# Performance work log

Hardware: AMD Instinct MI355X
Metric: run time of the kernel (lower is better)

Reference implementation:

```python
import jax, jax.numpy as jnp
import numpy as np

B, L, D, H = 4, 1024, 1024, 16
DH = D // H
NEG = -1e9


def setup_inputs() -> dict:
    key = jax.random.key(0)
    ks = jax.random.split(key, 8)
    sequence = jax.random.normal(ks[0], (B, L, D), dtype=jnp.float32)
    # additive padding mask: all tokens valid -> zeros
    padding_mask = jnp.zeros((B, 1, 1, L), dtype=jnp.float32)
    # additive causal dependency mask: -1e9 above the diagonal
    causal = jnp.triu(jnp.full((L, L), NEG, dtype=jnp.float32), k=1)
    dependency_mask = causal[None, None, :, :]
    scale = 1.0 / np.sqrt(D)
    Wq = jax.random.normal(ks[1], (D, D), dtype=jnp.float32) * scale
    Wk = jax.random.normal(ks[2], (D, D), dtype=jnp.float32) * scale
    Wv = jax.random.normal(ks[3], (D, D), dtype=jnp.float32) * scale
    bq = jnp.zeros((D,), dtype=jnp.float32)
    bk = jnp.zeros((D,), dtype=jnp.float32)
    bv = jnp.zeros((D,), dtype=jnp.float32)
    return {"sequence": sequence, "padding_mask": padding_mask,
            "dependency_mask": dependency_mask,
            "Wq": Wq, "bq": bq, "Wk": Wk, "bk": bk, "Wv": Wv, "bv": bv}


def reference(sequence, padding_mask, dependency_mask, Wq, bq, Wk, bk, Wv, bv):
    b, l, d = sequence.shape
    h, dh = H, d // H
    # Q/K/V linear projections (torch Linear: x @ W^T + b)
    q = (sequence @ Wq.T + bq).reshape(b, l, h, dh)
    k = (sequence @ Wk.T + bk).reshape(b, l, h, dh)
    v = (sequence @ Wv.T + bv).reshape(b, l, h, dh)
    # scaled dot-product scores: [B, H, L, L]
    scores = jnp.einsum('blhd,bmhd->bhlm', q, k) / jnp.sqrt(jnp.float32(dh))
    scores = scores + padding_mask + dependency_mask
    attn = jax.nn.softmax(scores, axis=-1)
    # dropout is identity in eval mode (training=False)
    out = jnp.einsum('bhlm,bmhd->blhd', attn, v)
    return out.reshape(b, l, d)
```

## Files before the change

kernel.cpp:

```cpp
#include <hip/hip_runtime.h>
#include <hip/hip_bf16.h>


#define LL 1024

typedef __attribute__((ext_vector_type(8))) short short8;
typedef __attribute__((ext_vector_type(4))) float floatx4;

__device__ __forceinline__ float bf2f(unsigned short u) {
    return __uint_as_float(((unsigned int)u) << 16);
}
__device__ __forceinline__ unsigned short f2bf(float f) {
    unsigned int x = __float_as_uint(f);
    unsigned int r = x + 0x7fffu + ((x >> 16) & 1u);
    return (unsigned short)(r >> 16);
}

#if __has_builtin(__builtin_amdgcn_global_load_lds)
#define HAVE_GLL 1
typedef __attribute__((address_space(1))) unsigned int as1_u32;
typedef __attribute__((address_space(3))) unsigned int as3_u32;
__device__ __forceinline__ void gll16(const void* g, void* l) {
    __builtin_amdgcn_global_load_lds((const as1_u32*)g, (as3_u32*)l, 16, 0, 0);
}
#endif

#if __has_builtin(__builtin_amdgcn_exp2f)
#define EXP2F(x) __builtin_amdgcn_exp2f(x)
#else
#define EXP2F(x) exp2f(x)
#endif

__global__ __launch_bounds__(256) void conv_in(
    const float* __restrict__ seq, const float* __restrict__ wq,
    const float* __restrict__ wk,  const float* __restrict__ wv,
    const float* __restrict__ bq,  const float* __restrict__ bk,
    const float* __restrict__ bv,  const float* __restrict__ pm,
    unsigned short* __restrict__ ws)
{
    unsigned int t = blockIdx.x * 256u + threadIdx.x;
    if (t >= 918400u) return;
    unsigned int e = t * 8u;
    const float* src; unsigned int idx; unsigned short* dst; float scale = 1.0f;
    if (e < 4194304u)      { src = seq; idx = e;            dst = ws + 12582912u; }
    else if (e < 5242880u) { src = wq;  idx = e - 4194304u; dst = ws + 16777216u; }
    else if (e < 6291456u) { src = wk;  idx = e - 5242880u; dst = ws + 17825792u; }
    else if (e < 7340032u) { src = wv;  idx = e - 6291456u; dst = ws + 18874368u; }
    else if (e < 7341056u) { src = bq;  idx = e - 7340032u; dst = ws + 20971520u; }
    else if (e < 7342080u) { src = bk;  idx = e - 7341056u; dst = ws + 20972544u; }
    else if (e < 7343104u) { src = bv;  idx = e - 7342080u; dst = ws + 20973568u; }
    else { src = pm; idx = e - 7343104u; dst = ws + 20974592u; scale = 1.4426950f; }
    float4 a = *(const float4*)(src + idx);
    float4 c = *(const float4*)(src + idx + 4);
    uint4 st;
    st.x = (unsigned)f2bf(a.x * scale) | ((unsigned)f2bf(a.y * scale) << 16);
    st.y = (unsigned)f2bf(a.z * scale) | ((unsigned)f2bf(a.w * scale) << 16);
    st.z = (unsigned)f2bf(c.x * scale) | ((unsigned)f2bf(c.y * scale) << 16);
    st.w = (unsigned)f2bf(c.z * scale) | ((unsigned)f2bf(c.w * scale) << 16);
    *(uint4*)(dst + idx) = st;
}

__global__ __launch_bounds__(512, 2) void qkv_proj(
    const unsigned short* __restrict__ X,
    const unsigned short* __restrict__ Wq, const unsigned short* __restrict__ bq,
    const unsigned short* __restrict__ Wk, const unsigned short* __restrict__ bk,
    const unsigned short* __restrict__ Wv, const unsigned short* __restrict__ bv,
    unsigned short* __restrict__ dst_base)
{
    const int z = blockIdx.z;
    const unsigned short* Wm   = (z == 0) ? Wq : ((z == 1) ? Wk : Wv);
    const unsigned short* bias = (z == 0) ? bq : ((z == 1) ? bk : bv);
    const float osc = (z == 0) ? 0.18033688f : 1.0f;
    unsigned short* dst = dst_base + (size_t)z * (4096u * 1024u);

    __shared__ __align__(16) unsigned short Abuf[2][16384];
    __shared__ __align__(16) unsigned short Bbuf[2][16384];

    const int tid  = threadIdx.x;
    const int lane = tid & 63;
    const int wave = tid >> 6;
    const int quad = lane >> 4, r16 = lane & 15;
    const int wr = wave >> 2, wc = wave & 3;
    const int m0 = blockIdx.x * 256;
    const int n0 = blockIdx.y * 256;

    const int r3   = lane >> 3;
    const int stc  = ((lane & 7) ^ r3) << 3;
    const int seg0 = wave * 4;

    const unsigned short* Asrc = X  + (size_t)(m0 + seg0 * 8 + r3) * 1024 + stc;
    const unsigned short* Bsrc = Wm + (size_t)(n0 + seg0 * 8 + r3) * 1024 + stc;

    floatx4 acc[8][4];
#pragma unroll
    for (int i = 0; i < 8; ++i)
#pragma unroll
        for (int j = 0; j < 4; ++j)
#pragma unroll
            for (int r = 0; r < 4; ++r) acc[i][j][r] = 0.f;

#ifdef HAVE_GLL
#pragma unroll
    for (int c = 0; c < 4; ++c) {
        gll16(Asrc + (size_t)c * 8192, &Abuf[0][(seg0 + c) * 512]);
        gll16(Bsrc + (size_t)c * 8192, &Bbuf[0][(seg0 + c) * 512]);
    }
#else
#pragma unroll
    for (int c = 0; c < 4; ++c) {
        *(uint4*)&Abuf[0][(seg0 + c) * 512 + lane * 8] = *(const uint4*)(Asrc + (size_t)c * 8192);
        *(uint4*)&Bbuf[0][(seg0 + c) * 512 + lane * 8] = *(const uint4*)(Bsrc + (size_t)c * 8192);
    }
#endif
    asm volatile("s_waitcnt vmcnt(0) lgkmcnt(0)" ::: "memory");
    __builtin_amdgcn_s_barrier();

#pragma unroll 2
    for (int t = 0; t < 16; ++t) {
        const int cur = t & 1;
        const int nxt = cur ^ 1;
        const int k0n = (t + 1) << 6;
        const unsigned short* Ac = Abuf[cur];
        const unsigned short* Bc = Bbuf[cur];
        const int arow = (wr * 128 + r16) * 64;
        const int brow = (wc * 64 + r16) * 64;
        const int c0 = ((0 + quad) ^ (r16 & 7)) << 3;
        const int c1 = ((4 + quad) ^ (r16 & 7)) << 3;
        short8 a[4], b[4];

#pragma unroll
        for (int i = 0; i < 4; ++i)
            a[i] = *(const short8*)&Ac[arow + i * 1024 + c0];
#pragma unroll
        for (int j = 0; j < 4; ++j)
            b[j] = *(const short8*)&Bc[brow + j * 1024 + c0];
        if (t < 15) {
#ifdef HAVE_GLL
#pragma unroll
            for (int c = 0; c < 4; ++c)
                gll16(Asrc + (size_t)c * 8192 + k0n, &Abuf[nxt][(seg0 + c) * 512]);
#else
#pragma unroll
            for (int c = 0; c < 4; ++c)
                *(uint4*)&Abuf[nxt][(seg0 + c) * 512 + lane * 8] =
                    *(const uint4*)(Asrc + (size_t)c * 8192 + k0n);
#endif
        }
        __builtin_amdgcn_s_barrier();
        asm volatile("s_waitcnt lgkmcnt(0)" ::: "memory");
        __builtin_amdgcn_s_setprio(1);
#pragma unroll
        for (int i = 0; i < 4; ++i)
#pragma unroll
            for (int j = 0; j < 4; ++j)
                acc[i][j] = __builtin_amdgcn_mfma_f32_16x16x32_bf16(a[i], b[j], acc[i][j], 0, 0, 0);
        __builtin_amdgcn_s_setprio(0);
        __builtin_amdgcn_s_barrier();

#pragma unroll
        for (int i = 0; i < 4; ++i)
            a[i] = *(const short8*)&Ac[arow + (4 + i) * 1024 + c0];
        if (t < 15) {
#ifdef HAVE_GLL
#pragma unroll
            for (int c = 0; c < 4; ++c)
                gll16(Bsrc + (size_t)c * 8192 + k0n, &Bbuf[nxt][(seg0 + c) * 512]);
#else
#pragma unroll
            for (int c = 0; c < 4; ++c)
                *(uint4*)&Bbuf[nxt][(seg0 + c) * 512 + lane * 8] =
                    *(const uint4*)(Bsrc + (size_t)c * 8192 + k0n);
#endif
        }
        __builtin_amdgcn_s_barrier();
        asm volatile("s_waitcnt lgkmcnt(0)" ::: "memory");
        __builtin_amdgcn_s_setprio(1);
#pragma unroll
        for (int i = 0; i < 4; ++i)
#pragma unroll
            for (int j = 0; j < 4; ++j)
                acc[4 + i][j] = __builtin_amdgcn_mfma_f32_16x16x32_bf16(a[i], b[j], acc[4 + i][j], 0, 0, 0);
        __builtin_amdgcn_s_setprio(0);
        __builtin_amdgcn_s_barrier();

#pragma unroll
        for (int i = 0; i < 4; ++i)
            a[i] = *(const short8*)&Ac[arow + i * 1024 + c1];
#pragma unroll
        for (int j = 0; j < 4; ++j)
            b[j] = *(const short8*)&Bc[brow + j * 1024 + c1];
        __builtin_amdgcn_s_barrier();
        asm volatile("s_waitcnt lgkmcnt(0)" ::: "memory");
        __builtin_amdgcn_s_setprio(1);
#pragma unroll
        for (int i = 0; i < 4; ++i)
#pragma unroll
            for (int j = 0; j < 4; ++j)
                acc[i][j] = __builtin_amdgcn_mfma_f32_16x16x32_bf16(a[i], b[j], acc[i][j], 0, 0, 0);
        __builtin_amdgcn_s_setprio(0);
        __builtin_amdgcn_s_barrier();

#pragma unroll
        for (int i = 0; i < 4; ++i)
            a[i] = *(const short8*)&Ac[arow + (4 + i) * 1024 + c1];
        __builtin_amdgcn_s_barrier();
        asm volatile("s_waitcnt lgkmcnt(0)" ::: "memory");
        __builtin_amdgcn_s_setprio(1);
#pragma unroll
        for (int i = 0; i < 4; ++i)
#pragma unroll
            for (int j = 0; j < 4; ++j)
                acc[4 + i][j] = __builtin_amdgcn_mfma_f32_16x16x32_bf16(a[i], b[j], acc[4 + i][j], 0, 0, 0);
        __builtin_amdgcn_s_setprio(0);
        if (t < 15) {
            asm volatile("s_waitcnt vmcnt(0) lgkmcnt(0)" ::: "memory");
        }
        __builtin_amdgcn_s_barrier();
    }

#pragma unroll
    for (int j = 0; j < 4; ++j) {
        int n = n0 + wc * 64 + j * 16 + r16;
        float bvf = bf2f(bias[n]);
        int h = n >> 6, d = n & 63;
#pragma unroll
        for (int i = 0; i < 8; ++i) {
            int m_base = m0 + wr * 128 + i * 16 + quad * 4;
            int b = m_base >> 10, l0 = m_base & 1023;
            if (z == 2) {
                ushort4 st;
                st.x = f2bf(acc[i][j][0] + bvf); st.y = f2bf(acc[i][j][1] + bvf);
                st.z = f2bf(acc[i][j][2] + bvf); st.w = f2bf(acc[i][j][3] + bvf);
                *(ushort4*)&dst[(((size_t)(b * 16 + h)) * 64 + d) * 1024 + l0] = st;
            } else {
#pragma unroll
                for (int r = 0; r < 4; ++r)
                    dst[(((size_t)(b * 16 + h)) * 1024 + (l0 + r)) * 64 + d] =
                        f2bf((acc[i][j][r] + bvf) * osc);
            }
        }
    }
}

__global__ __launch_bounds__(256) void attn(
    const unsigned short* __restrict__ Qw,
    const unsigned short* __restrict__ Kw,
    const unsigned short* __restrict__ Vt_g,
    const unsigned short* __restrict__ pmask,
    float* __restrict__ out)
{
    __shared__ __align__(16) unsigned short KsF[8192];
    __shared__ __align__(16) unsigned short VsF[8192];
    __shared__ __align__(16) unsigned short PsF[2][4][2048];

    const int tid  = threadIdx.x;
    const int lane = tid & 63;
    const int wave = tid >> 6;
    const int quad = lane >> 4, r16 = lane & 15;

    const int bid  = blockIdx.x;
    const int half = bid >> 8, idx = bid & 255;
    const int bh   = idx & 63;
    const int qb   = idx >> 6;
    const int qi   = half ? (7 - qb) : qb;
    const int b    = bh >> 4, h = bh & 15;
    const int q0   = qi << 7;

    const size_t base = (size_t)bh * (1024 * 64);
    const unsigned short* Qg = Qw + base;
    const unsigned short* Kg = Kw + base;
    const unsigned short* Vg = Vt_g + base;

    const int kst_r3  = lane >> 3;
    const int kst_col = ((lane & 7) ^ kst_r3) << 3;
    const int vst_r   = lane >> 4;

    short8 aq[2][2];
#pragma unroll
    for (int f = 0; f < 2; ++f) {
        int qrow = q0 + f * 64 + wave * 16 + r16;
        aq[f][0] = *(const short8*)(Qg + (size_t)qrow * 64 + quad * 8);
        aq[f][1] = *(const short8*)(Qg + (size_t)qrow * 64 + 32 + quad * 8);
    }

    short8 ones;
#pragma unroll
    for (int i = 0; i < 8; ++i) ones[i] = (short)0x3f80;

    floatx4 ol[2];
    floatx4 o[2][4];
#pragma unroll
    for (int f = 0; f < 2; ++f)
#pragma unroll
        for (int r = 0; r < 4; ++r) ol[f][r] = 0.f;
#pragma unroll
    for (int f = 0; f < 2; ++f)
#pragma unroll
        for (int j = 0; j < 4; ++j)
#pragma unroll
            for (int r = 0; r < 4; ++r) o[f][j][r] = 0.f;

    for (int kt = 0; kt <= qi; ++kt) {
        float pm2[8];
#pragma unroll
        for (int j = 0; j < 8; ++j)
            pm2[j] = bf2f(pmask[b * LL + kt * 128 + j * 16 + r16]) - 12.0f;

        __syncthreads();
#ifdef HAVE_GLL
#pragma unroll
        for (int c2 = 0; c2 < 4; ++c2) {
            int seg = wave * 4 + c2;
            int krow = seg * 8 + kst_r3;
            gll16(Kg + (size_t)(kt * 128 + krow) * 64 + kst_col, &KsF[seg * 512]);
            int vrow = seg * 4 + vst_r;
            int vcol = (((lane & 15) ^ (vrow & 7))) << 3;
            gll16(Vg + (size_t)vrow * 1024 + kt * 128 + vcol, &VsF[seg * 512]);
        }
#else
#pragma unroll
        for (int c2 = 0; c2 < 4; ++c2) {
            int seg = wave * 4 + c2;
            int krow = seg * 8 + kst_r3;
            *(uint4*)&KsF[seg * 512 + lane * 8] =
                *(const uint4*)(Kg + (size_t)(kt * 128 + krow) * 64 + kst_col);
            int vrow = seg * 4 + vst_r;
            int vcol = (((lane & 15) ^ (vrow & 7))) << 3;
            *(uint4*)&VsF[seg * 512 + lane * 8] =
                *(const uint4*)(Vg + (size_t)vrow * 1024 + kt * 128 + vcol);
        }
#endif
        __syncthreads();

#pragma unroll
        for (int f = 0; f < 2; ++f) {
            floatx4 s[8];
#pragma unroll
            for (int j = 0; j < 8; ++j)
#pragma unroll
                for (int r = 0; r < 4; ++r) s[j][r] = 0.f;
#pragma unroll
            for (int j = 0; j < 8; ++j) {
                short8 bk0 = *(const short8*)&KsF[(j * 16 + r16) * 64 + (((0 * 4 + quad) ^ (r16 & 7)) << 3)];
                s[j] = __builtin_amdgcn_mfma_f32_16x16x32_bf16(aq[f][0], bk0, s[j], 0, 0, 0);
                short8 bk1 = *(const short8*)&KsF[(j * 16 + r16) * 64 + (((1 * 4 + quad) ^ (r16 & 7)) << 3)];
                s[j] = __builtin_amdgcn_mfma_f32_16x16x32_bf16(aq[f][1], bk1, s[j], 0, 0, 0);
            }

            if (kt == qi) {
                const int my_q = q0 + f * 64 + wave * 16 + quad * 4;
#pragma unroll
                for (int j = 0; j < 8; ++j) {
                    int key = kt * 128 + j * 16 + r16;
#pragma unroll
                    for (int r = 0; r < 4; ++r)
                        if (key > my_q + r) s[j][r] -= 1.0e9f;
                }
            }

#pragma unroll
            for (int j = 0; j < 8; ++j) {
                int key = j * 16 + r16;
                int ab = ((key >> 5) << 9) + (((key >> 3) & 3) << 7) + (key & 7) + (quad << 5);
#pragma unroll
                for (int r = 0; r < 4; ++r) {
                    float p = EXP2F(s[j][r] + pm2[j]);
                    PsF[f][wave][ab + (r << 3)] = (unsigned short)(__float_as_uint(p) >> 16);
                }
            }
            asm volatile("s_waitcnt lgkmcnt(0)" ::: "memory");

#pragma unroll
            for (int kk4 = 0; kk4 < 4; ++kk4) {
                short8 ap = *(const short8*)&PsF[f][wave][kk4 * 512 + lane * 8];
                ol[f] = __builtin_amdgcn_mfma_f32_16x16x32_bf16(ap, ones, ol[f], 0, 0, 0);
#pragma unroll
                for (int j2 = 0; j2 < 4; ++j2) {
                    short8 bv = *(const short8*)&VsF[(j2 * 16 + r16) * 128 + (((kk4 * 4 + quad) ^ (r16 & 7)) << 3)];
                    o[f][j2] = __builtin_amdgcn_mfma_f32_16x16x32_bf16(ap, bv, o[f][j2], 0, 0, 0);
                }
            }
        }
    }

#pragma unroll
    for (int f = 0; f < 2; ++f) {
        float linv[4];
#pragma unroll
        for (int r = 0; r < 4; ++r)
            linv[r] = 1.0f / fmaxf(ol[f][r], 1.0e-30f);
        const int my_q = q0 + f * 64 + wave * 16 + quad * 4;
#pragma unroll
        for (int j2 = 0; j2 < 4; ++j2) {
            int d = j2 * 16 + r16;
#pragma unroll
            for (int r = 0; r < 4; ++r) {
                size_t oidx = ((size_t)(b * 1024 + my_q + r)) * 1024 + h * 64 + d;
                out[oidx] = o[f][j2][r] * linv[r];
            }
        }
    }
}

__global__ __launch_bounds__(256) void fill_sentinel_f(float* __restrict__ out,
                                                       float v, unsigned int n)
{
    unsigned int t = blockIdx.x * 256u + threadIdx.x;
    if (t < n) out[t] = v;
}

extern "C" void kernel_launch(void* const* d_in, const int* in_sizes, int n_in,
                              void* d_out, int out_size, void* d_ws, size_t ws_size,
                              hipStream_t stream) {
    bool sizes_ok = (n_in == 9) && in_sizes[0] == 4194304 && in_sizes[1] == 4096 &&
                    in_sizes[2] == 1048576 && in_sizes[3] == 1048576 && in_sizes[4] == 1024 &&
                    in_sizes[5] == 1048576 && in_sizes[6] == 1024 && in_sizes[7] == 1048576 &&
                    in_sizes[8] == 1024 && out_size == 4194304;
    if (!sizes_ok) {
        fill_sentinel_f<<<16384, 256, 0, stream>>>((float*)d_out, 100.0f, 4194304u);
        return;
    }
    if (ws_size < 50331652u) {
        fill_sentinel_f<<<16384, 256, 0, stream>>>((float*)d_out, 200.0f, 4194304u);
        return;
    }

    unsigned short* ws = (unsigned short*)d_ws;

    conv_in<<<3588, 256, 0, stream>>>(
        (const float*)d_in[0], (const float*)d_in[3], (const float*)d_in[5],
        (const float*)d_in[7], (const float*)d_in[4], (const float*)d_in[6],
        (const float*)d_in[8], (const float*)d_in[1], ws);

    const unsigned short* cseq = ws + 12582912u;
    const unsigned short* cwq  = ws + 16777216u;
    const unsigned short* cwk  = ws + 17825792u;
    const unsigned short* cwv  = ws + 18874368u;
    const unsigned short* cbq  = ws + 20971520u;
    const unsigned short* cbk  = ws + 20972544u;
    const unsigned short* cbv  = ws + 20973568u;
    const unsigned short* cpm  = ws + 20974592u;

    dim3 g1(16, 4, 3);
    qkv_proj<<<g1, 512, 0, stream>>>(cseq, cwq, cbq, cwk, cbk, cwv, cbv, ws);

    attn<<<512, 256, 0, stream>>>(ws, ws + 4194304u, ws + 8388608u, cpm, (float*)d_out);
}
```

Measured before the change: 157.0 us.

## Fuse QKV weights into one GEMM with 256x192 tiles and triple-buffered A

The Q, K and V weights and biases, already contiguous in the workspace, are treated as one 3072-wide weight matrix. The projection now runs as a single GEMM on a 16x16 grid of 256x192 tiles, replacing the 16x4x3 grid of 256x256 tiles, so it launches 256 blocks instead of 192 and fills the CUs more evenly. The A operand moves to a three-stage LDS ring that prefetches two K-steps ahead, with partial vmcnt waits, so global loads overlap more with MFMA work. The epilogue works out Q/K/V per column and applies each one's scale and output layout, which adds a branch per column group. Each tile also does less MFMA work per A load, and the new wait counts must match the number of loads in flight.

```diff
diff --git a/kernel.cpp b/kernel.cpp
--- a/kernel.cpp
+++ b/kernel.cpp
@@ -62,19 +62,12 @@
 
 __global__ __launch_bounds__(512, 2) void qkv_proj(
     const unsigned short* __restrict__ X,
-    const unsigned short* __restrict__ Wq, const unsigned short* __restrict__ bq,
-    const unsigned short* __restrict__ Wk, const unsigned short* __restrict__ bk,
-    const unsigned short* __restrict__ Wv, const unsigned short* __restrict__ bv,
+    const unsigned short* __restrict__ Wcat,
+    const unsigned short* __restrict__ bcat,
     unsigned short* __restrict__ dst_base)
 {
-    const int z = blockIdx.z;
-    const unsigned short* Wm   = (z == 0) ? Wq : ((z == 1) ? Wk : Wv);
-    const unsigned short* bias = (z == 0) ? bq : ((z == 1) ? bk : bv);
-    const float osc = (z == 0) ? 0.18033688f : 1.0f;
-    unsigned short* dst = dst_base + (size_t)z * (4096u * 1024u);
-
-    __shared__ __align__(16) unsigned short Abuf[2][16384];
-    __shared__ __align__(16) unsigned short Bbuf[2][16384];
+    __shared__ __align__(16) unsigned short Abuf[3][16384];
+    __shared__ __align__(16) unsigned short Bbuf[2][12288];
 
     const int tid  = threadIdx.x;
     const int lane = tid & 63;
@@ -82,161 +75,175 @@
     const int quad = lane >> 4, r16 = lane & 15;
     const int wr = wave >> 2, wc = wave & 3;
     const int m0 = blockIdx.x * 256;
-    const int n0 = blockIdx.y * 256;
+    const int n0 = blockIdx.y * 192;
 
     const int r3   = lane >> 3;
     const int stc  = ((lane & 7) ^ r3) << 3;
-    const int seg0 = wave * 4;
-
-    const unsigned short* Asrc = X  + (size_t)(m0 + seg0 * 8 + r3) * 1024 + stc;
-    const unsigned short* Bsrc = Wm + (size_t)(n0 + seg0 * 8 + r3) * 1024 + stc;
-
-    floatx4 acc[8][4];
+    const int seg0a = wave * 4;
+    const int seg0b = wave * 3;
+
+    const unsigned short* Asrc = X    + (size_t)(m0 + seg0a * 8 + r3) * 1024 + stc;
+    const unsigned short* Bsrc = Wcat + (size_t)(n0 + seg0b * 8 + r3) * 1024 + stc;
+
+    floatx4 acc[8][3];
 #pragma unroll
     for (int i = 0; i < 8; ++i)
 #pragma unroll
-        for (int j = 0; j < 4; ++j)
+        for (int j = 0; j < 3; ++j)
 #pragma unroll
             for (int r = 0; r < 4; ++r) acc[i][j][r] = 0.f;
 
 #ifdef HAVE_GLL
 #pragma unroll
-    for (int c = 0; c < 4; ++c) {
-        gll16(Asrc + (size_t)c * 8192, &Abuf[0][(seg0 + c) * 512]);
-        gll16(Bsrc + (size_t)c * 8192, &Bbuf[0][(seg0 + c) * 512]);
-    }
-#else
-#pragma unroll
-    for (int c = 0; c < 4; ++c) {
-        *(uint4*)&Abuf[0][(seg0 + c) * 512 + lane * 8] = *(const uint4*)(Asrc + (size_t)c * 8192);
-        *(uint4*)&Bbuf[0][(seg0 + c) * 512 + lane * 8] = *(const uint4*)(Bsrc + (size_t)c * 8192);
-    }
-#endif
-    asm volatile("s_waitcnt vmcnt(0) lgkmcnt(0)" ::: "memory");
+    for (int c = 0; c < 4; ++c) gll16(Asrc + (size_t)c * 8192, &Abuf[0][(seg0a + c) * 512]);
+#pragma unroll
+    for (int c = 0; c < 3; ++c) gll16(Bsrc + (size_t)c * 8192, &Bbuf[0][(seg0b + c) * 512]);
+#pragma unroll
+    for (int c = 0; c < 4; ++c) gll16(Asrc + (size_t)c * 8192 + 64, &Abuf[1][(seg0a + c) * 512]);
+    asm volatile("s_waitcnt vmcnt(4)" ::: "memory");
     __builtin_amdgcn_s_barrier();
-
-#pragma unroll 2
+#endif
+
+    int sA = 0;
     for (int t = 0; t < 16; ++t) {
-        const int cur = t & 1;
-        const int nxt = cur ^ 1;
-        const int k0n = (t + 1) << 6;
-        const unsigned short* Ac = Abuf[cur];
-        const unsigned short* Bc = Bbuf[cur];
-        const int arow = (wr * 128 + r16) * 64;
-        const int brow = (wc * 64 + r16) * 64;
+        const unsigned short* Ac = &Abuf[sA][0];
+        const unsigned short* Bc = &Bbuf[t & 1][0];
+        const int aoff = (wr * 128 + r16) * 64;
+        const int boff = (wc * 48 + r16) * 64;
         const int c0 = ((0 + quad) ^ (r16 & 7)) << 3;
         const int c1 = ((4 + quad) ^ (r16 & 7)) << 3;
-        short8 a[4], b[4];
-
+        short8 a[4], b[3];
+
+#ifndef HAVE_GLL
+        __syncthreads();
+#pragma unroll
+        for (int c = 0; c < 4; ++c)
+            *(uint4*)&Abuf[0][(seg0a + c) * 512 + lane * 8] =
+                *(const uint4*)(Asrc + (size_t)c * 8192 + (t << 6));
+#pragma unroll
+        for (int c = 0; c < 3; ++c)
+            *(uint4*)&Bbuf[0][(seg0b + c) * 512 + lane * 8] =
+                *(const uint4*)(Bsrc + (size_t)c * 8192 + (t << 6));
+        __syncthreads();
+        Ac = &Abuf[0][0]; Bc = &Bbuf[0][0];
+#endif
+
+#pragma unroll
+        for (int i = 0; i < 4; ++i) a[i] = *(const short8*)&Ac[aoff + i * 1024 + c0];
+#pragma unroll
+        for (int j = 0; j < 3; ++j) b[j] = *(const short8*)&Bc[boff + j * 1024 + c0];
+#ifdef HAVE_GLL
+        if (t < 15) {
+            const int sBw = (t + 1) & 1;
+            const size_t ko = (size_t)((t + 1) << 6);
+#pragma unroll
+            for (int c = 0; c < 3; ++c)
+                gll16(Bsrc + (size_t)c * 8192 + ko, &Bbuf[sBw][(seg0b + c) * 512]);
+        }
+        __builtin_amdgcn_s_barrier();
+        asm volatile("s_waitcnt lgkmcnt(0)" ::: "memory");
+#endif
+        __builtin_amdgcn_s_setprio(1);
 #pragma unroll
         for (int i = 0; i < 4; ++i)
-            a[i] = *(const short8*)&Ac[arow + i * 1024 + c0];
-#pragma unroll
-        for (int j = 0; j < 4; ++j)
-            b[j] = *(const short8*)&Bc[brow + j * 1024 + c0];
-        if (t < 15) {
-#ifdef HAVE_GLL
-#pragma unroll
-            for (int c = 0; c < 4; ++c)
-                gll16(Asrc + (size_t)c * 8192 + k0n, &Abuf[nxt][(seg0 + c) * 512]);
-#else
-#pragma unroll
-            for (int c = 0; c < 4; ++c)
-                *(uint4*)&Abuf[nxt][(seg0 + c) * 512 + lane * 8] =
-                    *(const uint4*)(Asrc + (size_t)c * 8192 + k0n);
-#endif
-        }
-        __builtin_amdgcn_s_barrier();
-        asm volatile("s_waitcnt lgkmcnt(0)" ::: "memory");
-        __builtin_amdgcn_s_setprio(1);
-#pragma unroll
-        for (int i = 0; i < 4; ++i)
-#pragma unroll
-            for (int j = 0; j < 4; ++j)
+#pragma unroll
+            for (int j = 0; j < 3; ++j)
                 acc[i][j] = __builtin_amdgcn_mfma_f32_16x16x32_bf16(a[i], b[j], acc[i][j], 0, 0, 0);
         __builtin_amdgcn_s_setprio(0);
-        __builtin_amdgcn_s_barrier();
-
+#ifdef HAVE_GLL
+        __builtin_amdgcn_s_barrier();
+#endif
+
+#pragma unroll
+        for (int i = 0; i < 4; ++i) a[i] = *(const short8*)&Ac[aoff + (4 + i) * 1024 + c0];
+#ifdef HAVE_GLL
+        if (t < 14) {
+            const int sAw = (sA == 0) ? 2 : (sA - 1);
+            const size_t ko = (size_t)((t + 2) << 6);
+#pragma unroll
+            for (int c = 0; c < 4; ++c)
+                gll16(Asrc + (size_t)c * 8192 + ko, &Abuf[sAw][(seg0a + c) * 512]);
+        }
+        __builtin_amdgcn_s_barrier();
+        asm volatile("s_waitcnt lgkmcnt(0)" ::: "memory");
+#endif
+        __builtin_amdgcn_s_setprio(1);
 #pragma unroll
         for (int i = 0; i < 4; ++i)
-            a[i] = *(const short8*)&Ac[arow + (4 + i) * 1024 + c0];
-        if (t < 15) {
-#ifdef HAVE_GLL
-#pragma unroll
-            for (int c = 0; c < 4; ++c)
-                gll16(Bsrc + (size_t)c * 8192 + k0n, &Bbuf[nxt][(seg0 + c) * 512]);
-#else
-#pragma unroll
-            for (int c = 0; c < 4; ++c)
-                *(uint4*)&Bbuf[nxt][(seg0 + c) * 512 + lane * 8] =
-                    *(const uint4*)(Bsrc + (size_t)c * 8192 + k0n);
-#endif
-        }
-        __builtin_amdgcn_s_barrier();
-        asm volatile("s_waitcnt lgkmcnt(0)" ::: "memory");
-        __builtin_amdgcn_s_setprio(1);
-#pragma unroll
-        for (int i = 0; i < 4; ++i)
-#pragma unroll
-            for (int j = 0; j < 4; ++j)
+#pragma unroll
+            for (int j = 0; j < 3; ++j)
                 acc[4 + i][j] = __builtin_amdgcn_mfma_f32_16x16x32_bf16(a[i], b[j], acc[4 + i][j], 0, 0, 0);
         __builtin_amdgcn_s_setprio(0);
-        __builtin_amdgcn_s_barrier();
-
+#ifdef HAVE_GLL
+        __builtin_amdgcn_s_barrier();
+#endif
+
+#pragma unroll
+        for (int i = 0; i < 4; ++i) a[i] = *(const short8*)&Ac[aoff + i * 1024 + c1];
+#pragma unroll
+        for (int j = 0; j < 3; ++j) b[j] = *(const short8*)&Bc[boff + j * 1024 + c1];
+#ifdef HAVE_GLL
+        __builtin_amdgcn_s_barrier();
+        asm volatile("s_waitcnt lgkmcnt(0)" ::: "memory");
+#endif
+        __builtin_amdgcn_s_setprio(1);
 #pragma unroll
         for (int i = 0; i < 4; ++i)
-            a[i] = *(const short8*)&Ac[arow + i * 1024 + c1];
-#pragma unroll
-        for (int j = 0; j < 4; ++j)
-            b[j] = *(const short8*)&Bc[brow + j * 1024 + c1];
-        __builtin_amdgcn_s_barrier();
-        asm volatile("s_waitcnt lgkmcnt(0)" ::: "memory");
-        __builtin_amdgcn_s_setprio(1);
-#pragma unroll
-        for (int i = 0; i < 4; ++i)
-#pragma unroll
-            for (int j = 0; j < 4; ++j)
+#pragma unroll
+            for (int j = 0; j < 3; ++j)
                 acc[i][j] = __builtin_amdgcn_mfma_f32_16x16x32_bf16(a[i], b[j], acc[i][j], 0, 0, 0);
         __builtin_amdgcn_s_setprio(0);
-        __builtin_amdgcn_s_barrier();
-
+#ifdef HAVE_GLL
+        __builtin_amdgcn_s_barrier();
+#endif
+
+#pragma unroll
+        for (int i = 0; i < 4; ++i) a[i] = *(const short8*)&Ac[aoff + (4 + i) * 1024 + c1];
+#ifdef HAVE_GLL
+        __builtin_amdgcn_s_barrier();
+        asm volatile("s_waitcnt lgkmcnt(0)" ::: "memory");
+#endif
+        __builtin_amdgcn_s_setprio(1);
 #pragma unroll
         for (int i = 0; i < 4; ++i)
-            a[i] = *(const short8*)&Ac[arow + (4 + i) * 1024 + c1];
-        __builtin_amdgcn_s_barrier();
-        asm volatile("s_waitcnt lgkmcnt(0)" ::: "memory");
-        __builtin_amdgcn_s_setprio(1);
-#pragma unroll
-        for (int i = 0; i < 4; ++i)
-#pragma unroll
-            for (int j = 0; j < 4; ++j)
+#pragma unroll
+            for (int j = 0; j < 3; ++j)
                 acc[4 + i][j] = __builtin_amdgcn_mfma_f32_16x16x32_bf16(a[i], b[j], acc[4 + i][j], 0, 0, 0);
         __builtin_amdgcn_s_setprio(0);
-        if (t < 15) {
-            asm volatile("s_waitcnt vmcnt(0) lgkmcnt(0)" ::: "memory");
-        }
-        __builtin_amdgcn_s_barrier();
-    }
-
-#pragma unroll
-    for (int j = 0; j < 4; ++j) {
-        int n = n0 + wc * 64 + j * 16 + r16;
-        float bvf = bf2f(bias[n]);
-        int h = n >> 6, d = n & 63;
+#ifdef HAVE_GLL
+        if (t < 14) {
+            asm volatile("s_waitcnt vmcnt(4)" ::: "memory");
+        } else if (t == 14) {
+            asm volatile("s_waitcnt vmcnt(0)" ::: "memory");
+        }
+        __builtin_amdgcn_s_barrier();
+#endif
+        sA = (sA == 2) ? 0 : (sA + 1);
+    }
+
+#pragma unroll
+    for (int j = 0; j < 3; ++j) {
+        int n = n0 + wc * 48 + j * 16 + r16;
+        int z = n >> 10;
+        int nn = n & 1023;
+        float bvf = bf2f(bcat[n]);
+        float sc = (z == 0) ? 0.18033688f : 1.0f;
+        int h = nn >> 6, d = nn & 63;
+        unsigned short* dst = dst_base + (size_t)z * (4096u * 1024u);
 #pragma unroll
         for (int i = 0; i < 8; ++i) {
             int m_base = m0 + wr * 128 + i * 16 + quad * 4;
-            int b = m_base >> 10, l0 = m_base & 1023;
+            int bb = m_base >> 10, l0 = m_base & 1023;
             if (z == 2) {
                 ushort4 st;
                 st.x = f2bf(acc[i][j][0] + bvf); st.y = f2bf(acc[i][j][1] + bvf);
                 st.z = f2bf(acc[i][j][2] + bvf); st.w = f2bf(acc[i][j][3] + bvf);
-                *(ushort4*)&dst[(((size_t)(b * 16 + h)) * 64 + d) * 1024 + l0] = st;
+                *(ushort4*)&dst[(((size_t)(bb * 16 + h)) * 64 + d) * 1024 + l0] = st;
             } else {
 #pragma unroll
                 for (int r = 0; r < 4; ++r)
-                    dst[(((size_t)(b * 16 + h)) * 1024 + (l0 + r)) * 64 + d] =
-                        f2bf((acc[i][j][r] + bvf) * osc);
+                    dst[(((size_t)(bb * 16 + h)) * 1024 + (l0 + r)) * 64 + d] =
+                        f2bf((acc[i][j][r] + bvf) * sc);
             }
         }
     }
@@ -432,17 +439,13 @@
         (const float*)d_in[7], (const float*)d_in[4], (const float*)d_in[6],
         (const float*)d_in[8], (const float*)d_in[1], ws);
 
-    const unsigned short* cseq = ws + 12582912u;
-    const unsigned short* cwq  = ws + 16777216u;
-    const unsigned short* cwk  = ws + 17825792u;
-    const unsigned short* cwv  = ws + 18874368u;
-    const unsigned short* cbq  = ws + 20971520u;
-    const unsigned short* cbk  = ws + 20972544u;
-    const unsigned short* cbv  = ws + 20973568u;
-    const unsigned short* cpm  = ws + 20974592u;
-
-    dim3 g1(16, 4, 3);
-    qkv_proj<<<g1, 512, 0, stream>>>(cseq, cwq, cbq, cwk, cbk, cwv, cbv, ws);
+    const unsigned short* cseq  = ws + 12582912u;
+    const unsigned short* cwcat = ws + 16777216u;
+    const unsigned short* cbcat = ws + 20971520u;
+    const unsigned short* cpm   = ws + 20974592u;
+
+    dim3 g1(16, 16);
+    qkv_proj<<<g1, 512, 0, stream>>>(cseq, cwcat, cbcat, ws);
 
     attn<<<512, 256, 0, stream>>>(ws, ws + 4194304u, ws + 8388608u, cpm, (float*)d_out);
 }
```

After: 150.1 us. 4.3% less time.
